# Optimization experiments

Measured on AMD Instinct MI355X. Metric: run time of the kernel, lower is better.

## Reference

```python
import jax, jax.numpy as jnp
import numpy as np

EPS = 1e-3  # keras LayerNormalization default epsilon


def layer_norm(x, g, b):
    mu = jnp.mean(x, axis=-1, keepdims=True)
    var = jnp.mean(jnp.square(x - mu), axis=-1, keepdims=True)
    return g * (x - mu) / jnp.sqrt(var + EPS) + b


def setup_inputs() -> dict:
    key = jax.random.key(0)
    ks = jax.random.split(key, 16)
    B, S, E, H, F = 2, 4096, 512, 8, 2048
    s_e = 1.0 / np.sqrt(E)
    s_f = 1.0 / np.sqrt(F)
    inp = {
        "x": jax.random.normal(ks[0], (B, S, E), dtype=jnp.float32),
        "WQ": jax.random.normal(ks[1], (E, E), dtype=jnp.float32) * s_e,
        "bQ": jnp.zeros((E,), jnp.float32),
        "WK": jax.random.normal(ks[2], (E, E), dtype=jnp.float32) * s_e,
        "bK": jnp.zeros((E,), jnp.float32),
        "WV": jax.random.normal(ks[3], (E, E), dtype=jnp.float32) * s_e,
        "bV": jnp.zeros((E,), jnp.float32),
        "WO": jax.random.normal(ks[4], (E, E), dtype=jnp.float32) * s_e,
        "bO": jnp.zeros((E,), jnp.float32),
        "W1": jax.random.normal(ks[5], (E, F), dtype=jnp.float32) * s_e,
        "b1": jnp.zeros((F,), jnp.float32),
        "W2": jax.random.normal(ks[6], (F, E), dtype=jnp.float32) * s_f,
        "b2": jnp.zeros((E,), jnp.float32),
        "g1": jnp.ones((E,), jnp.float32),
        "beta1": jnp.zeros((E,), jnp.float32),
        "g2": jnp.ones((E,), jnp.float32),
        "beta2": jnp.zeros((E,), jnp.float32),
        "num_head": 8,
    }
    return inp


def reference(x, WQ, bQ, WK, bK, WV, bV, WO, bO, W1, b1, W2, b2,
              g1, beta1, g2, beta2, num_head):
    B, S, E = x.shape
    H = num_head
    d = E // H
    scale = jnp.sqrt(jnp.asarray(d, jnp.float32))

    q = (x @ WQ + bQ).reshape(B, S, H, d).transpose(0, 2, 1, 3)  # [B,H,S,d]
    k = (x @ WK + bK).reshape(B, S, H, d).transpose(0, 2, 1, 3)
    v = (x @ WV + bV).reshape(B, S, H, d).transpose(0, 2, 1, 3)

    score = jnp.einsum('bhqd,bhkd->bhqk', q, k) / scale  # O(S^2) materialized, as in source
    attn = jax.nn.softmax(score, axis=-1)
    zs = jnp.einsum('bhqk,bhkd->bhqd', attn, v)  # [B,H,S,d]

    # Faithful to source bug: reshape [B,H,S,d] -> [B,S,E] WITHOUT transposing back
    zs = zs.reshape(B, S, E)
    zs = zs @ WO + bO

    z = layer_norm(zs + x, g1, beta1)
    r = jax.nn.relu(z @ W1 + b1) @ W2 + b2
    r = layer_norm(r + z, g2, beta2)
    return r
```

## Files before the change

kernel.cpp:

```cpp
#include <hip/hip_runtime.h>
#include <hip/hip_bf16.h>

typedef unsigned short u16;
typedef __attribute__((ext_vector_type(8))) short bf16x8;
typedef __attribute__((ext_vector_type(4))) float f32x4;
typedef __attribute__((ext_vector_type(16))) float f32x16;

static constexpr int BB = 2;
static constexpr int SS = 4096;
static constexpr int EE = 512;
static constexpr int HH = 8;
static constexpr int DD = 64;
static constexpr int FF = 2048;
static constexpr int NR = BB * SS;
static constexpr int QS = 3 * EE;

#define QSCALE 0.18033688011112042f

__device__ __forceinline__ u16 f2bf(float f) {
  union { float f; unsigned u; } v; v.f = f;
  unsigned r = v.u + 0x7FFFu + ((v.u >> 16) & 1u);
  return (u16)(r >> 16);
}
__device__ __forceinline__ unsigned pack2(float a, float b) {
  return (unsigned)f2bf(a) | ((unsigned)f2bf(b) << 16);
}
__device__ __forceinline__ float bf2f_lo(unsigned u) {
  union { unsigned u; float f; } v; v.u = u << 16; return v.f;
}
__device__ __forceinline__ float bf2f_hi(unsigned u) {
  union { unsigned u; float f; } v; v.u = u & 0xffff0000u; return v.f;
}
__device__ __forceinline__ unsigned cvtpk(float lo, float hi) {
  unsigned r;
  asm("v_cvt_pk_bf16_f32 %0, %1, %2" : "=v"(r) : "v"(lo), "v"(hi));
  return r;
}
__device__ __forceinline__ void perm32swap(unsigned& a, unsigned& b) {
  asm("v_permlane32_swap_b32 %0, %1" : "+v"(a), "+v"(b));
}
__device__ __forceinline__ void gload_lds16(const u16* g, u16* l) {
  __builtin_amdgcn_global_load_lds(
      (const __attribute__((address_space(1))) unsigned*)g,
      (__attribute__((address_space(3))) unsigned*)l, 16, 0, 0);
}

struct TrJob { const float* W; u16* Wt; int K, N, k0, n0; };

__device__ __forceinline__ void transp_tile(const float* W, u16* Wt, int K,
                                            int N, int k0, int n0, int t) {
  __shared__ float T[64][65];
  const int tn = t & 63, tk = t >> 6;
#pragma unroll
  for (int i = 0; i < 16; ++i) {
    int kk = tk * 16 + i;
    T[kk][tn] = W[(size_t)(k0 + kk) * N + n0 + tn];
  }
  __syncthreads();
#pragma unroll
  for (int i = 0; i < 16; ++i) {
    int nn = tk * 16 + i;
    Wt[(size_t)(n0 + nn) * K + k0 + tn] = f2bf(T[tn][nn]);
  }
}

__global__ __launch_bounds__(256) void prep_all(
    const float* __restrict__ x, u16* __restrict__ xb,
    const float* __restrict__ WQ, const float* __restrict__ WK,
    const float* __restrict__ WV, const float* __restrict__ WO,
    const float* __restrict__ W1, const float* __restrict__ W2,
    u16* __restrict__ Wqkv_t, u16* __restrict__ WO_t, u16* __restrict__ W1_t,
    u16* __restrict__ W2_t, const float* __restrict__ bQ,
    const float* __restrict__ bK, const float* __restrict__ bV,
    float* __restrict__ bqkv) {
  const int bx = blockIdx.x;
  const int t = threadIdx.x;
  if (bx < 2048) {
    int i = (bx * 256 + t) * 8;
    float4 a = *(const float4*)(x + i);
    float4 b = *(const float4*)(x + i + 4);
    uint4 u;
    u.x = pack2(a.x, a.y); u.y = pack2(a.z, a.w);
    u.z = pack2(b.x, b.y); u.w = pack2(b.z, b.w);
    *(uint4*)(xb + i) = u;
    return;
  }
  int idx = bx - 2048;
  if (idx < 768) {
    TrJob j;
    if (idx < 256) {
      const float* srcs[4] = {WQ, WK, WV, WO};
      u16* dsts[4] = {Wqkv_t, Wqkv_t + 512 * 512, Wqkv_t + 1024 * 512, WO_t};
      int w = idx >> 6, l = idx & 63;
      j = {srcs[w], dsts[w], 512, 512, (l & 7) * 64, (l >> 3) * 64};
    } else if (idx < 512) {
      int l = idx - 256;
      j = {W1, W1_t, 512, 2048, (l & 7) * 64, (l >> 3) * 64};
    } else {
      int l = idx - 512;
      j = {W2, W2_t, 2048, 512, (l & 31) * 64, (l >> 5) * 64};
    }
    transp_tile(j.W, j.Wt, j.K, j.N, j.k0, j.n0, t);
    return;
  }
  for (int i = t; i < QS; i += 256)
    bqkv[i] = i < 512 ? bQ[i] : (i < 1024 ? bK[i - 512] : bV[i - 1024]);
}

__global__ __launch_bounds__(256) void transp_v(const u16* __restrict__ qkvb,
                                                u16* __restrict__ vt) {
  __shared__ u16 T[64][72];
  const int s0 = blockIdx.x * 64, c0 = blockIdx.y * 64, b = blockIdx.z;
  const int t = threadIdx.x;
#pragma unroll
  for (int i = 0; i < 2; ++i) {
    int idx = t + i * 256;
    int row = idx >> 3, c8 = idx & 7;
    *(uint4*)(&T[row][c8 * 8]) = *(const uint4*)(
        &qkvb[((size_t)b * SS + s0 + row) * QS + 1024 + c0 + c8 * 8]);
  }
  __syncthreads();
#pragma unroll
  for (int i = 0; i < 2; ++i) {
    int idx = t + i * 256;
    int c = idx >> 3, s8 = idx & 7;
    u16 tmp[8];
#pragma unroll
    for (int j = 0; j < 8; ++j) tmp[j] = T[s8 * 8 + j][c];
    *(uint4*)(&vt[((size_t)b * EE + c0 + c) * SS + s0 + s8 * 8]) =
        *(uint4*)tmp;
  }
}

template <int RELU, int OUT_BF16, int SCALEQ = 0>
__global__ __launch_bounds__(256) void gemm64(
    const u16* __restrict__ A, const u16* __restrict__ Bt,
    const float* __restrict__ bias, void* __restrict__ Cout,
    int M, int N, int K) {
  __shared__ __align__(16) u16 As[2][64 * 64];
  __shared__ __align__(16) u16 Bs[2][64 * 64];
  const int t = threadIdx.x;
  const int lane = t & 63, wid = t >> 6;
  const int lm = lane & 15, lg = lane >> 4;
  const int bm = blockIdx.x * 64, bn = blockIdx.y * 64;
  const int wr = (wid >> 1) * 32, wc = (wid & 1) * 32;
  const int sr = lane >> 3;
  const int scb = (lane & 7) ^ sr;

  f32x4 acc[2][2];
#pragma unroll
  for (int i = 0; i < 2; ++i)
#pragma unroll
    for (int j = 0; j < 2; ++j) acc[i][j] = (f32x4){0.f, 0.f, 0.f, 0.f};

  auto stage = [&](int kb, int buf) {
#pragma unroll
    for (int i = 0; i < 2; ++i) {
      int r8 = wid * 16 + i * 8;
      gload_lds16(A + (size_t)(bm + r8 + sr) * K + kb + scb * 8,
                  &As[buf][r8 * 64]);
      gload_lds16(Bt + (size_t)(bn + r8 + sr) * K + kb + scb * 8,
                  &Bs[buf][r8 * 64]);
    }
  };

  stage(0, 0);
  const int nsteps = K >> 6;
  for (int s = 0; s < nsteps; ++s) {
    const int cur = s & 1;
    __syncthreads();
    if (s + 1 < nsteps) stage((s + 1) << 6, cur ^ 1);

#pragma unroll
    for (int c = 0; c < 2; ++c) {
      bf16x8 af[2], bfr[2];
#pragma unroll
      for (int i = 0; i < 2; ++i) {
        int ar = wr + i * 16 + lm;
        af[i] = *(const bf16x8*)(
            &As[cur][ar * 64 + (((c * 4 + lg) ^ (ar & 7)) << 3)]);
        int br = wc + i * 16 + lm;
        bfr[i] = *(const bf16x8*)(
            &Bs[cur][br * 64 + (((c * 4 + lg) ^ (br & 7)) << 3)]);
      }
#pragma unroll
      for (int i = 0; i < 2; ++i)
#pragma unroll
        for (int j = 0; j < 2; ++j)
          acc[i][j] = __builtin_amdgcn_mfma_f32_16x16x32_bf16(
              af[i], bfr[j], acc[i][j], 0, 0, 0);
    }
  }

  float bi[2];
#pragma unroll
  for (int j = 0; j < 2; ++j) bi[j] = bias[bn + wc + j * 16 + lm];

#pragma unroll
  for (int i = 0; i < 2; ++i) {
#pragma unroll
    for (int j = 0; j < 2; ++j) {
      int col = bn + wc + j * 16 + lm;
#pragma unroll
      for (int r = 0; r < 4; ++r) {
        int row = bm + wr + i * 16 + lg * 4 + r;
        float vv = acc[i][j][r] + bi[j];
        if (RELU) vv = fmaxf(vv, 0.f);
        if (SCALEQ && col < 512) vv *= QSCALE;
        if (OUT_BF16)
          ((u16*)Cout)[(size_t)row * N + col] = f2bf(vv);
        else
          ((float*)Cout)[(size_t)row * N + col] = vv;
      }
    }
  }
}

__global__ __launch_bounds__(128) void attn_mfma(
    const u16* __restrict__ qkv, const u16* __restrict__ vt,
    u16* __restrict__ zs) {
  __shared__ __align__(16) u16 K_lds[2][64 * 64];
  __shared__ __align__(16) u16 V_lds[2][64 * 64];
  __shared__ float Linv[2][32];

  const int qblock = blockIdx.x;
  const int bh = blockIdx.y;
  const int b = bh >> 3, h = bh & 7;
  const int t = threadIdx.x;
  const int lane = t & 63, wid = t >> 6;
  const int q32 = lane & 31, hi = lane >> 5;
  const int qs7 = q32 & 7;
  const size_t bS = (size_t)b * SS;
  const int qbase = qblock * 64 + wid * 32;

  bf16x8 qf[4];
  {
    const u16* qrow = qkv + (bS + qbase + q32) * QS + h * DD + hi * 8;
#pragma unroll
    for (int c = 0; c < 4; ++c) qf[c] = *(const bf16x8*)(qrow + c * 16);
  }

  const int sr = lane >> 3;
  const int scb = (lane & 7) ^ sr;

  const u16* kcur = qkv + 512 + bS * QS + h * DD;
  const u16* vcur = vt + ((size_t)b * EE + h * DD) * SS;
  size_t koff[4], voff[4];
#pragma unroll
  for (int i = 0; i < 4; ++i) {
    int rbase = wid * 32 + i * 8 + sr;
    koff[i] = (size_t)rbase * QS + scb * 8;
    voff[i] = (size_t)rbase * SS + scb * 8;
  }

  f32x16 o0, o1;
#pragma unroll
  for (int i = 0; i < 16; ++i) { o0[i] = 0.f; o1[i] = 0.f; }
  float lsum = 0.f;

  auto stage = [&](int bufi) {
#pragma unroll
    for (int i = 0; i < 4; ++i) {
      int rbase = wid * 32 + i * 8;
      gload_lds16(kcur + koff[i], &K_lds[bufi][rbase * 64]);
      gload_lds16(vcur + voff[i], &V_lds[bufi][rbase * 64]);
    }
  };

  stage(0);

  for (int kt = 0; kt < SS / 64; ++kt) {
    const int cur = kt & 1;
    __syncthreads();
    if (kt + 1 < SS / 64) {
      kcur += 64 * QS;
      vcur += 64;
      stage(cur ^ 1);
    }

    auto qk = [&](int blk) -> f32x16 {
      f32x16 s;
#pragma unroll
      for (int i = 0; i < 16; ++i) s[i] = 0.f;
      const int krow = blk * 32 + q32;
      __builtin_amdgcn_s_setprio(1);
#pragma unroll
      for (int c = 0; c < 4; ++c) {
        bf16x8 kf = *(const bf16x8*)(
            &K_lds[cur][krow * 64 + (((2 * c + hi) ^ qs7) << 3)]);
        s = __builtin_amdgcn_mfma_f32_32x32x16_bf16(kf, qf[c], s, 0, 0, 0);
      }
      __builtin_amdgcn_s_setprio(0);
      return s;
    };
    auto pv = [&](const float* p, int kc) {
      const int rA = (kc & 1) * 8, rB = rA + 4;
      unsigned wA0 = cvtpk(p[rA + 0], p[rA + 1]);
      unsigned wA1 = cvtpk(p[rA + 2], p[rA + 3]);
      unsigned wB0 = cvtpk(p[rB + 0], p[rB + 1]);
      unsigned wB1 = cvtpk(p[rB + 2], p[rB + 3]);
      perm32swap(wA0, wB0);
      perm32swap(wA1, wB1);
      union { unsigned u[4]; bf16x8 v; } pf;
      pf.u[0] = wA0; pf.u[1] = wA1; pf.u[2] = wB0; pf.u[3] = wB1;
      bf16x8 vf0 = *(const bf16x8*)(
          &V_lds[cur][q32 * 64 + (((2 * kc + hi) ^ qs7) << 3)]);
      bf16x8 vf1 = *(const bf16x8*)(
          &V_lds[cur][(32 + q32) * 64 + (((2 * kc + hi) ^ qs7) << 3)]);
      __builtin_amdgcn_s_setprio(1);
      o0 = __builtin_amdgcn_mfma_f32_32x32x16_bf16(pf.v, vf0, o0, 0, 0, 0);
      o1 = __builtin_amdgcn_mfma_f32_32x32x16_bf16(pf.v, vf1, o1, 0, 0, 0);
      __builtin_amdgcn_s_setprio(0);
    };

    f32x16 s0 = qk(0);
    float p0[16];
#pragma unroll
    for (int r = 0; r < 16; ++r) {
      p0[r] = __builtin_amdgcn_exp2f(s0[r]);
      lsum += p0[r];
    }
    f32x16 s1 = qk(1);
    pv(p0, 0);
    pv(p0, 1);
    float p1[16];
#pragma unroll
    for (int r = 0; r < 16; ++r) {
      p1[r] = __builtin_amdgcn_exp2f(s1[r]);
      lsum += p1[r];
    }
    pv(p1, 2);
    pv(p1, 3);
  }

  float fl = lsum + __shfl_xor(lsum, 32);
  if (lane < 32) Linv[wid][q32] = 1.f / fl;

#pragma unroll
  for (int reg = 0; reg < 16; ++reg) {
    int q = (reg & 3) + 8 * (reg >> 2) + 4 * hi;
    float inv = Linv[wid][q];
    int s = qbase + q;
    u16* dst = zs + ((size_t)b * SS + h * 512 + (s >> 3)) * EE + (s & 7) * 64;
    dst[q32] = f2bf(o0[reg] * inv);
    dst[32 + q32] = f2bf(o1[reg] * inv);
  }
}

template <int WF32>
__global__ __launch_bounds__(128) void add_ln_b(
    const u16* __restrict__ a, const u16* __restrict__ xres,
    const float* __restrict__ g, const float* __restrict__ beta,
    u16* __restrict__ outb, float* __restrict__ outf) {
  const int row = blockIdx.x;
  const int tid = threadIdx.x;
  uint2 av = *(const uint2*)(a + (size_t)row * EE + tid * 4);
  uint2 xv = *(const uint2*)(xres + (size_t)row * EE + tid * 4);
  float vx = bf2f_lo(av.x) + bf2f_lo(xv.x);
  float vy = bf2f_hi(av.x) + bf2f_hi(xv.x);
  float vz = bf2f_lo(av.y) + bf2f_lo(xv.y);
  float vw = bf2f_hi(av.y) + bf2f_hi(xv.y);
  float sum = vx + vy + vz + vw;
  float sq = vx * vx + vy * vy + vz * vz + vw * vw;
#pragma unroll
  for (int off = 1; off < 64; off <<= 1) {
    sum += __shfl_xor(sum, off);
    sq += __shfl_xor(sq, off);
  }
  __shared__ float s0[2], s1[2];
  int w = tid >> 6;
  if ((tid & 63) == 0) { s0[w] = sum; s1[w] = sq; }
  __syncthreads();
  sum = s0[0] + s0[1];
  sq = s1[0] + s1[1];
  float mu = sum * (1.0f / EE);
  float var = sq * (1.0f / EE) - mu * mu;
  float r = rsqrtf(var + 1e-3f);
  int c = tid * 4;
  float4 gv = *(const float4*)(g + c);
  float4 bv = *(const float4*)(beta + c);
  float o0 = gv.x * (vx - mu) * r + bv.x;
  float o1 = gv.y * (vy - mu) * r + bv.y;
  float o2 = gv.z * (vz - mu) * r + bv.z;
  float o3 = gv.w * (vw - mu) * r + bv.w;
  if (WF32) {
    float4 ov = {o0, o1, o2, o3};
    *(float4*)(outf + (size_t)row * EE + c) = ov;
  } else {
    uint2 u;
    u.x = pack2(o0, o1);
    u.y = pack2(o2, o3);
    *(uint2*)(outb + (size_t)row * EE + c) = u;
  }
}

extern "C" void kernel_launch(void* const* d_in, const int* in_sizes, int n_in,
                              void* d_out, int out_size, void* d_ws,
                              size_t ws_size, hipStream_t stream) {
  const float* x = (const float*)d_in[0];
  const float* WQ = (const float*)d_in[1];
  const float* bQ = (const float*)d_in[2];
  const float* WK = (const float*)d_in[3];
  const float* bK = (const float*)d_in[4];
  const float* WV = (const float*)d_in[5];
  const float* bV = (const float*)d_in[6];
  const float* WO = (const float*)d_in[7];
  const float* bO = (const float*)d_in[8];
  const float* W1 = (const float*)d_in[9];
  const float* b1 = (const float*)d_in[10];
  const float* W2 = (const float*)d_in[11];
  const float* b2 = (const float*)d_in[12];
  const float* g1 = (const float*)d_in[13];
  const float* be1 = (const float*)d_in[14];
  const float* g2 = (const float*)d_in[15];
  const float* be2 = (const float*)d_in[16];
  float* out = (float*)d_out;

  const size_t MB = 1u << 20;
  char* w = (char*)d_ws;
  u16* Wqkv_t = (u16*)(w + 0);
  u16* WO_t   = (u16*)(w + 2 * MB);
  u16* W1_t   = (u16*)(w + 3 * MB);
  u16* W2_t   = (u16*)(w + 5 * MB);
  float* bqkv = (float*)(w + 7 * MB);
  u16* qkvb = (u16*)(w + 8 * MB);
  u16* zsb  = (u16*)(w + 32 * MB);
  u16* zs2b = (u16*)(w + 40 * MB);
  u16* f2b  = (u16*)(w + 48 * MB);
  u16* zb   = (u16*)(w + 72 * MB);
  u16* xb   = (u16*)(w + 80 * MB);
  u16* vtb  = (u16*)(w + 88 * MB);
  u16* f1   = (u16*)(w + 8 * MB);

  dim3 blk(256);

  prep_all<<<dim3(2817), blk, 0, stream>>>(x, xb, WQ, WK, WV, WO, W1, W2,
                                           Wqkv_t, WO_t, W1_t, W2_t, bQ, bK,
                                           bV, bqkv);

  gemm64<0, 1, 1><<<dim3(128, 24), blk, 0, stream>>>(xb, Wqkv_t, bqkv, qkvb,
                                                     NR, QS, EE);
  transp_v<<<dim3(SS / 64, EE / 64, BB), blk, 0, stream>>>(qkvb, vtb);
  attn_mfma<<<dim3(SS / 64, BB * HH), dim3(128), 0, stream>>>(qkvb, vtb, zsb);
  gemm64<0, 1><<<dim3(128, 8), blk, 0, stream>>>(zsb, WO_t, bO, zs2b,
                                                 NR, EE, EE);
  add_ln_b<0><<<dim3(NR), dim3(128), 0, stream>>>(zs2b, xb, g1, be1, zb,
                                                  nullptr);
  gemm64<1, 1><<<dim3(128, 32), blk, 0, stream>>>(zb, W1_t, b1, f1,
                                                  NR, FF, EE);
  gemm64<0, 1><<<dim3(128, 8), blk, 0, stream>>>(f1, W2_t, b2, f2b,
                                                 NR, EE, FF);
  add_ln_b<1><<<dim3(NR), dim3(128), 0, stream>>>(f2b, zb, g2, be2, nullptr,
                                                  out);
}
```

Measured before the change: 228.2 us.

## Rework attention K/V pipeline with explicit vmcnt waits and swap grid order

The attention kernel now issues the next K/V tile load first, then waits with an explicit s_waitcnt vmcnt(8) and a raw s_barrier instead of __syncthreads, so only the current tile's loads must land. It computes both QK blocks and exps before all four PV MFMAs, under a single raised priority, and adds a trailing barrier to protect the buffer. The grid is transposed so consecutive blocks share the same query block across heads, which changes L2 locality, and per-thread precomputed offsets are replaced by recomputed addresses. Risks include correctness of the hand-written waitcnt counts and higher register pressure from holding both probability blocks.

```diff
diff --git a/kernel.cpp b/kernel.cpp
--- a/kernel.cpp
+++ b/kernel.cpp
@@ -223,14 +223,16 @@
   __shared__ __align__(16) u16 V_lds[2][64 * 64];
   __shared__ float Linv[2][32];
 
-  const int qblock = blockIdx.x;
-  const int bh = blockIdx.y;
+  const int bh = blockIdx.x;
+  const int qblock = blockIdx.y;
   const int b = bh >> 3, h = bh & 7;
   const int t = threadIdx.x;
   const int lane = t & 63, wid = t >> 6;
   const int q32 = lane & 31, hi = lane >> 5;
   const int qs7 = q32 & 7;
   const size_t bS = (size_t)b * SS;
+  const u16* kp = qkv + 512;
+  const u16* vrow = vt + ((size_t)b * EE + h * DD) * SS;
   const int qbase = qblock * 64 + wid * 32;
 
   bf16x8 qf[4];
@@ -243,42 +245,39 @@
   const int sr = lane >> 3;
   const int scb = (lane & 7) ^ sr;
 
-  const u16* kcur = qkv + 512 + bS * QS + h * DD;
-  const u16* vcur = vt + ((size_t)b * EE + h * DD) * SS;
-  size_t koff[4], voff[4];
-#pragma unroll
-  for (int i = 0; i < 4; ++i) {
-    int rbase = wid * 32 + i * 8 + sr;
-    koff[i] = (size_t)rbase * QS + scb * 8;
-    voff[i] = (size_t)rbase * SS + scb * 8;
-  }
-
   f32x16 o0, o1;
 #pragma unroll
   for (int i = 0; i < 16; ++i) { o0[i] = 0.f; o1[i] = 0.f; }
   float lsum = 0.f;
 
-  auto stage = [&](int bufi) {
+  auto stage = [&](int kt, int bufi) {
 #pragma unroll
     for (int i = 0; i < 4; ++i) {
       int rbase = wid * 32 + i * 8;
-      gload_lds16(kcur + koff[i], &K_lds[bufi][rbase * 64]);
-      gload_lds16(vcur + voff[i], &V_lds[bufi][rbase * 64]);
+      gload_lds16(kp + (bS + kt * 64 + rbase + sr) * QS + h * DD + scb * 8,
+                  &K_lds[bufi][rbase * 64]);
+      gload_lds16(vrow + (size_t)(rbase + sr) * SS + kt * 64 + scb * 8,
+                  &V_lds[bufi][rbase * 64]);
     }
   };
 
-  stage(0);
-
-  for (int kt = 0; kt < SS / 64; ++kt) {
+  stage(0, 0);
+
+  constexpr int NT = SS / 64;
+  for (int kt = 0; kt < NT; ++kt) {
     const int cur = kt & 1;
-    __syncthreads();
-    if (kt + 1 < SS / 64) {
-      kcur += 64 * QS;
-      vcur += 64;
-      stage(cur ^ 1);
-    }
-
-    auto qk = [&](int blk) -> f32x16 {
+    if (kt + 1 < NT) {
+      stage(kt + 1, cur ^ 1);
+      asm volatile("s_waitcnt vmcnt(8)" ::: "memory");
+    } else {
+      asm volatile("s_waitcnt vmcnt(0)" ::: "memory");
+    }
+    __builtin_amdgcn_sched_barrier(0);
+    __builtin_amdgcn_s_barrier();
+
+    float p[2][16];
+#pragma unroll
+    for (int blk = 0; blk < 2; ++blk) {
       f32x16 s;
 #pragma unroll
       for (int i = 0; i < 16; ++i) s[i] = 0.f;
@@ -291,14 +290,21 @@
         s = __builtin_amdgcn_mfma_f32_32x32x16_bf16(kf, qf[c], s, 0, 0, 0);
       }
       __builtin_amdgcn_s_setprio(0);
-      return s;
-    };
-    auto pv = [&](const float* p, int kc) {
-      const int rA = (kc & 1) * 8, rB = rA + 4;
-      unsigned wA0 = cvtpk(p[rA + 0], p[rA + 1]);
-      unsigned wA1 = cvtpk(p[rA + 2], p[rA + 3]);
-      unsigned wB0 = cvtpk(p[rB + 0], p[rB + 1]);
-      unsigned wB1 = cvtpk(p[rB + 2], p[rB + 3]);
+#pragma unroll
+      for (int r = 0; r < 16; ++r) {
+        p[blk][r] = __builtin_amdgcn_exp2f(s[r]);
+        lsum += p[blk][r];
+      }
+    }
+
+    __builtin_amdgcn_s_setprio(1);
+#pragma unroll
+    for (int kc = 0; kc < 4; ++kc) {
+      const int bb = kc >> 1, rA = (kc & 1) * 8, rB = rA + 4;
+      unsigned wA0 = cvtpk(p[bb][rA + 0], p[bb][rA + 1]);
+      unsigned wA1 = cvtpk(p[bb][rA + 2], p[bb][rA + 3]);
+      unsigned wB0 = cvtpk(p[bb][rB + 0], p[bb][rB + 1]);
+      unsigned wB1 = cvtpk(p[bb][rB + 2], p[bb][rB + 3]);
       perm32swap(wA0, wB0);
       perm32swap(wA1, wB1);
       union { unsigned u[4]; bf16x8 v; } pf;
@@ -307,30 +313,13 @@
           &V_lds[cur][q32 * 64 + (((2 * kc + hi) ^ qs7) << 3)]);
       bf16x8 vf1 = *(const bf16x8*)(
           &V_lds[cur][(32 + q32) * 64 + (((2 * kc + hi) ^ qs7) << 3)]);
-      __builtin_amdgcn_s_setprio(1);
       o0 = __builtin_amdgcn_mfma_f32_32x32x16_bf16(pf.v, vf0, o0, 0, 0, 0);
       o1 = __builtin_amdgcn_mfma_f32_32x32x16_bf16(pf.v, vf1, o1, 0, 0, 0);
-      __builtin_amdgcn_s_setprio(0);
-    };
-
-    f32x16 s0 = qk(0);
-    float p0[16];
-#pragma unroll
-    for (int r = 0; r < 16; ++r) {
-      p0[r] = __builtin_amdgcn_exp2f(s0[r]);
-      lsum += p0[r];
-    }
-    f32x16 s1 = qk(1);
-    pv(p0, 0);
-    pv(p0, 1);
-    float p1[16];
-#pragma unroll
-    for (int r = 0; r < 16; ++r) {
-      p1[r] = __builtin_amdgcn_exp2f(s1[r]);
-      lsum += p1[r];
-    }
-    pv(p1, 2);
-    pv(p1, 3);
+    }
+    __builtin_amdgcn_s_setprio(0);
+
+    asm volatile("s_waitcnt lgkmcnt(0)" ::: "memory");
+    __builtin_amdgcn_s_barrier();
   }
 
   float fl = lsum + __shfl_xor(lsum, 32);
@@ -441,7 +430,7 @@
   gemm64<0, 1, 1><<<dim3(128, 24), blk, 0, stream>>>(xb, Wqkv_t, bqkv, qkvb,
                                                      NR, QS, EE);
   transp_v<<<dim3(SS / 64, EE / 64, BB), blk, 0, stream>>>(qkvb, vtb);
-  attn_mfma<<<dim3(SS / 64, BB * HH), dim3(128), 0, stream>>>(qkvb, vtb, zsb);
+  attn_mfma<<<dim3(BB * HH, SS / 64), dim3(128), 0, stream>>>(qkvb, vtb, zsb);
   gemm64<0, 1><<<dim3(128, 8), blk, 0, stream>>>(zsb, WO_t, bO, zs2b,
                                                  NR, EE, EE);
   add_ln_b<0><<<dim3(NR), dim3(128), 0, stream>>>(zs2b, xb, g1, be1, zb,
```

New measurement: 217.1 us. 1.05x faster.
